# Kernel tuning notes

Measured on AMD Instinct MI355X. Metric: run time of the kernel, lower is better.

Reference implementation:

```python
import jax, jax.numpy as jnp
import numpy as np

B = 131072      # tokens routed (e.g., 16 seqs x 8192 tokens)
D_MODEL = 768
N_EXPERTS = 8
TOP_K = 2


def setup_inputs() -> dict:
    key = jax.random.key(0)
    k_h, k_w, k_b = jax.random.split(key, 3)
    h = jax.random.normal(k_h, (B, D_MODEL), dtype=jnp.float32)
    gate_w = jax.random.normal(k_w, (N_EXPERTS, D_MODEL), dtype=jnp.float32) * 0.02
    gate_b = jax.random.normal(k_b, (N_EXPERTS,), dtype=jnp.float32) * 0.02
    return {"h": h, "gate_w": gate_w, "gate_b": gate_b}


def reference(h, gate_w, gate_b):
    # gate projection: [B, d_model] @ [d_model, n_experts] + bias -> [B, n_experts]
    logits = jnp.einsum("bd,ed->be", h, gate_w) + gate_b
    # top-k selection (values, indices), then softmax over the top-k logits
    topk_vals, topk_idx = jax.lax.top_k(logits, TOP_K)   # [B, top_k] each
    weights = jax.nn.softmax(topk_vals, axis=-1)          # [B, top_k]
    return (topk_idx, weights)
```

## Files before the change

### kernel.cpp

```cpp
#include <hip/hip_runtime.h>


#define B_TOKENS 131072
#define DM 768
#define NE 8
#define TAU 1e-4f

__global__ __launch_bounds__(256) void router_main(
    const float* __restrict__ h,
    const float* __restrict__ gw,
    const float* __restrict__ gb,
    float* __restrict__ out,
    unsigned char* __restrict__ flags)
{
    const int lane = threadIdx.x & 63;
    const int wid = (blockIdx.x * blockDim.x + threadIdx.x) >> 6;
    const int n_waves = (gridDim.x * blockDim.x) >> 6;

    float wf[NE][3][4];
#pragma unroll
    for (int e = 0; e < NE; ++e)
#pragma unroll
        for (int g = 0; g < 3; ++g) {
            const float4 v = *reinterpret_cast<const float4*>(
                &gw[e * DM + g * 256 + lane * 4]);
            wf[e][g][0] = v.x; wf[e][g][1] = v.y;
            wf[e][g][2] = v.z; wf[e][g][3] = v.w;
        }

    float biasf[NE];
#pragma unroll
    for (int e = 0; e < NE; ++e) biasf[e] = gb[e];

    const bool hi32 = (lane & 32) != 0;
    const bool hi16 = (lane & 16) != 0;
    const bool hi8  = (lane & 8)  != 0;

    for (int t = wid; t < B_TOKENS; t += n_waves) {
        const float* hr = h + (size_t)t * DM;
        float4 buf[3];
#pragma unroll
        for (int g = 0; g < 3; ++g)
            buf[g] = *reinterpret_cast<const float4*>(&hr[g * 256 + lane * 4]);

        float accf[NE] = {0, 0, 0, 0, 0, 0, 0, 0};
#pragma unroll
        for (int g = 0; g < 3; ++g) {
            const float* bp = reinterpret_cast<const float*>(&buf[g]);
#pragma unroll
            for (int j = 0; j < 4; ++j) {
                const float hv = bp[j];
#pragma unroll
                for (int e = 0; e < NE; ++e)
                    accf[e] = fmaf(hv, wf[e][g][j], accf[e]);
            }
        }

        float r4[4];
#pragma unroll
        for (int j = 0; j < 4; ++j) {
            const float give = hi32 ? accf[j] : accf[4 + j];
            const float keep = hi32 ? accf[4 + j] : accf[j];
            r4[j] = keep + __shfl_xor(give, 32);
        }
        float r2[2];
#pragma unroll
        for (int j = 0; j < 2; ++j) {
            const float give = hi16 ? r4[j] : r4[2 + j];
            const float keep = hi16 ? r4[2 + j] : r4[j];
            r2[j] = keep + __shfl_xor(give, 16);
        }
        const float give = hi8 ? r2[0] : r2[1];
        const float keep = hi8 ? r2[1] : r2[0];
        float v = keep + __shfl_xor(give, 8);
        v += __shfl_xor(v, 4);
        v += __shfl_xor(v, 2);
        v += __shfl_xor(v, 1);

        float lg[NE];
#pragma unroll
        for (int e = 0; e < NE; ++e)
            lg[e] = __shfl(v, (e << 3) | (lane & 7)) + biasf[e];

        int i0 = 0; float v0 = lg[0];
#pragma unroll
        for (int e = 1; e < NE; ++e)
            if (lg[e] > v0) { v0 = lg[e]; i0 = e; }
        int i1 = -1; float v1 = -3.4e38f;
#pragma unroll
        for (int e = 0; e < NE; ++e)
            if (e != i0 && lg[e] > v1) { v1 = lg[e]; i1 = e; }
        float v2 = -3.4e38f;
#pragma unroll
        for (int e = 0; e < NE; ++e)
            if (e != i0 && e != i1 && lg[e] > v2) v2 = lg[e];

        const bool amb = (v0 - v1 < TAU) || (v1 - v2 < TAU);

        const float ex = expf(v1 - v0);
        const float w1 = ex / (1.0f + ex);
        const float w0 = 1.0f - w1;

        if (lane == 0) {
            *reinterpret_cast<float2*>(&out[2 * (size_t)t]) =
                make_float2((float)i0, (float)i1);
            *reinterpret_cast<float2*>(
                &out[2 * (size_t)B_TOKENS + 2 * (size_t)t]) =
                make_float2(w0, w1);
            flags[t] = amb ? 1 : 0;
        }
    }
}

__global__ __launch_bounds__(256) void router_repair(
    const float* __restrict__ h,
    const float* __restrict__ gw,
    const float* __restrict__ gb,
    float* __restrict__ out,
    const unsigned char* __restrict__ flags)
{
    const int lane = threadIdx.x & 63;
    const int w = (blockIdx.x * blockDim.x + threadIdx.x) >> 6;
    const int t0 = w * 64;
    if (t0 >= B_TOKENS) return;

    const unsigned char f = flags[t0 + lane];
    unsigned long long mask = __ballot(f != 0);
    if (mask == 0ull) return;

    float wf[NE][3][4];
#pragma unroll
    for (int e = 0; e < NE; ++e)
#pragma unroll
        for (int g = 0; g < 3; ++g) {
            const float4 vv = *reinterpret_cast<const float4*>(
                &gw[e * DM + g * 256 + lane * 4]);
            wf[e][g][0] = vv.x; wf[e][g][1] = vv.y;
            wf[e][g][2] = vv.z; wf[e][g][3] = vv.w;
        }
    double biasd[NE];
#pragma unroll
    for (int e = 0; e < NE; ++e) biasd[e] = (double)gb[e];

    const bool hi32 = (lane & 32) != 0;
    const bool hi16 = (lane & 16) != 0;
    const bool hi8  = (lane & 8)  != 0;

    while (mask) {
        const int p = __ffsll(mask) - 1;
        mask &= (mask - 1);
        const int t = t0 + p;

        const float* hr = h + (size_t)t * DM;
        float4 buf[3];
#pragma unroll
        for (int g = 0; g < 3; ++g)
            buf[g] = *reinterpret_cast<const float4*>(&hr[g * 256 + lane * 4]);

        double acc[NE] = {0, 0, 0, 0, 0, 0, 0, 0};
#pragma unroll
        for (int g = 0; g < 3; ++g) {
            const float* bp = reinterpret_cast<const float*>(&buf[g]);
#pragma unroll
            for (int j = 0; j < 4; ++j) {
                const double hd = (double)bp[j];
#pragma unroll
                for (int e = 0; e < NE; ++e)
                    acc[e] = fma(hd, (double)wf[e][g][j], acc[e]);
            }
        }
        double d4[4];
#pragma unroll
        for (int j = 0; j < 4; ++j) {
            const double give = hi32 ? acc[j] : acc[4 + j];
            const double keep = hi32 ? acc[4 + j] : acc[j];
            d4[j] = keep + __shfl_xor(give, 32);
        }
        double d2[2];
#pragma unroll
        for (int j = 0; j < 2; ++j) {
            const double give = hi16 ? d4[j] : d4[2 + j];
            const double keep = hi16 ? d4[2 + j] : d4[j];
            d2[j] = keep + __shfl_xor(give, 16);
        }
        const double give = hi8 ? d2[0] : d2[1];
        const double keep = hi8 ? d2[1] : d2[0];
        double dv = keep + __shfl_xor(give, 8);
        dv += __shfl_xor(dv, 4);
        dv += __shfl_xor(dv, 2);
        dv += __shfl_xor(dv, 1);

        double dlg[NE];
#pragma unroll
        for (int e = 0; e < NE; ++e)
            dlg[e] = __shfl(dv, (e << 3) | (lane & 7)) + biasd[e];

        int i0 = 0; double dv0 = dlg[0];
#pragma unroll
        for (int e = 1; e < NE; ++e)
            if (dlg[e] > dv0) { dv0 = dlg[e]; i0 = e; }
        int i1 = (i0 == 0) ? 1 : 0; double dv1 = dlg[i1];
#pragma unroll
        for (int e = 0; e < NE; ++e)
            if (e != i0 && dlg[e] > dv1) { dv1 = dlg[e]; i1 = e; }

        const float ex = expf((float)(dv1 - dv0));
        const float w1 = ex / (1.0f + ex);
        const float w0 = 1.0f - w1;

        if (lane == 0) {
            *reinterpret_cast<float2*>(&out[2 * (size_t)t]) =
                make_float2((float)i0, (float)i1);
            *reinterpret_cast<float2*>(
                &out[2 * (size_t)B_TOKENS + 2 * (size_t)t]) =
                make_float2(w0, w1);
        }
    }
}

extern "C" void kernel_launch(void* const* d_in, const int* in_sizes, int n_in,
                              void* d_out, int out_size, void* d_ws, size_t ws_size,
                              hipStream_t stream) {
    const float* h  = (const float*)d_in[0];
    const float* gw = (const float*)d_in[1];
    const float* gb = (const float*)d_in[2];
    float* out = (float*)d_out;
    unsigned char* flags = (unsigned char*)d_ws;

    router_main<<<dim3(2048), dim3(256), 0, stream>>>(h, gw, gb, out, flags);
    router_repair<<<dim3(512), dim3(256), 0, stream>>>(h, gw, gb, out, flags);
}
```

Baseline: 103.9 us.

## Restructure router to one token per thread with async LDS triple-buffered loads

The main kernel now assigns one token per thread instead of one token per wave. Each block streams its 256 token rows through a triple-buffered LDS ring using global_load_lds DMA, and gate weights are staged in LDS. Because each thread holds a token's full dot products, the cross-lane shuffle reductions are gone and every thread writes its own output. This adds a large LDS footprint (about 60KB), which limits occupancy, plus per-chunk barriers, and relies on hand-written vmcnt waits being correct.

```diff
diff --git a/kernel.cpp b/kernel.cpp
--- a/kernel.cpp
+++ b/kernel.cpp
@@ -5,6 +5,17 @@
 #define DM 768
 #define NE 8
 #define TAU 1e-4f
+#define TPB 256
+#define CH 12
+#define NCH 64
+#define HBUF 3072
+
+typedef const __attribute__((address_space(1))) void* gbl_vp;
+typedef __attribute__((address_space(3))) void* lds_vp;
+
+__device__ __forceinline__ void dma16(const float* g, float* l) {
+    __builtin_amdgcn_global_load_lds((gbl_vp)g, (lds_vp)l, 16, 0, 0);
+}
 
 __global__ __launch_bounds__(256) void router_main(
     const float* __restrict__ h,
@@ -13,103 +24,109 @@
     float* __restrict__ out,
     unsigned char* __restrict__ flags)
 {
-    const int lane = threadIdx.x & 63;
-    const int wid = (blockIdx.x * blockDim.x + threadIdx.x) >> 6;
-    const int n_waves = (gridDim.x * blockDim.x) >> 6;
-
-    float wf[NE][3][4];
+    __shared__ __align__(16) float w_lds[NE * DM];
+    __shared__ __align__(16) float h_lds[3 * HBUF];
+
+    const int tid  = threadIdx.x;
+    const int lane = tid & 63;
+    const int wv   = __builtin_amdgcn_readfirstlane(tid >> 6);
+    const int tb   = blockIdx.x * TPB;
+
+    const float* src[3];
+#pragma unroll
+    for (int i = 0; i < 3; ++i) {
+        const int sigma = wv * 192 + i * 64 + lane;
+        const int r = sigma / 3, g = sigma % 3;
+        src[i] = h + (size_t)(tb + r) * DM + g * 4;
+    }
+    const int dstoff0 = wv * 768;
+
+    dma16(src[0], &h_lds[0 * HBUF + dstoff0 + 0]);
+    dma16(src[1], &h_lds[0 * HBUF + dstoff0 + 256]);
+    dma16(src[2], &h_lds[0 * HBUF + dstoff0 + 512]);
+#pragma unroll
+    for (int i = 0; i < 3; ++i)
+        dma16(src[i] + CH, &h_lds[1 * HBUF + dstoff0 + i * 256]);
+#pragma unroll
+    for (int i = 0; i < 3; ++i) src[i] += 2 * CH;
+
+#pragma unroll
+    for (int s = 0; s < 6; ++s) {
+        const float4 v = *reinterpret_cast<const float4*>(&gw[(tid + s * TPB) * 4]);
+        *reinterpret_cast<float4*>(&w_lds[(tid + s * TPB) * 4]) = v;
+    }
+    float bias[NE];
+#pragma unroll
+    for (int e = 0; e < NE; ++e) bias[e] = gb[e];
+
+    __syncthreads();
+
+    float acc[NE] = {0, 0, 0, 0, 0, 0, 0, 0};
+
+    for (int k = 0; k < NCH; ++k) {
+        if (k == NCH - 1) {
+            asm volatile("s_waitcnt vmcnt(0)" ::: "memory");
+        } else {
+            asm volatile("s_waitcnt vmcnt(3)" ::: "memory");
+        }
+        __builtin_amdgcn_s_barrier();
+        __builtin_amdgcn_sched_barrier(0);
+
+        if (k + 2 < NCH) {
+            float* dst = &h_lds[((k + 2) % 3) * HBUF + dstoff0];
+            dma16(src[0], dst);
+            dma16(src[1], dst + 256);
+            dma16(src[2], dst + 512);
+#pragma unroll
+            for (int i = 0; i < 3; ++i) src[i] += CH;
+        }
+        __builtin_amdgcn_sched_barrier(0);
+
+        const float* row = &h_lds[(k % 3) * HBUF + tid * CH];
+        const int wbase = k * CH;
+#pragma unroll
+        for (int g2 = 0; g2 < 3; ++g2) {
+            const float4 hv = *reinterpret_cast<const float4*>(&row[g2 * 4]);
+#pragma unroll
+            for (int e = 0; e < NE; ++e) {
+                const float4 wv4 = *reinterpret_cast<const float4*>(
+                    &w_lds[e * DM + wbase + g2 * 4]);
+                acc[e] = fmaf(hv.x, wv4.x, acc[e]);
+                acc[e] = fmaf(hv.y, wv4.y, acc[e]);
+                acc[e] = fmaf(hv.z, wv4.z, acc[e]);
+                acc[e] = fmaf(hv.w, wv4.w, acc[e]);
+            }
+        }
+    }
+
+    float lg[NE];
+#pragma unroll
+    for (int e = 0; e < NE; ++e) lg[e] = acc[e] + bias[e];
+
+    int i0 = 0; float v0 = lg[0];
+#pragma unroll
+    for (int e = 1; e < NE; ++e)
+        if (lg[e] > v0) { v0 = lg[e]; i0 = e; }
+    int i1 = -1; float v1 = -3.4e38f;
 #pragma unroll
     for (int e = 0; e < NE; ++e)
-#pragma unroll
-        for (int g = 0; g < 3; ++g) {
-            const float4 v = *reinterpret_cast<const float4*>(
-                &gw[e * DM + g * 256 + lane * 4]);
-            wf[e][g][0] = v.x; wf[e][g][1] = v.y;
-            wf[e][g][2] = v.z; wf[e][g][3] = v.w;
-        }
-
-    float biasf[NE];
-#pragma unroll
-    for (int e = 0; e < NE; ++e) biasf[e] = gb[e];
-
-    const bool hi32 = (lane & 32) != 0;
-    const bool hi16 = (lane & 16) != 0;
-    const bool hi8  = (lane & 8)  != 0;
-
-    for (int t = wid; t < B_TOKENS; t += n_waves) {
-        const float* hr = h + (size_t)t * DM;
-        float4 buf[3];
-#pragma unroll
-        for (int g = 0; g < 3; ++g)
-            buf[g] = *reinterpret_cast<const float4*>(&hr[g * 256 + lane * 4]);
-
-        float accf[NE] = {0, 0, 0, 0, 0, 0, 0, 0};
-#pragma unroll
-        for (int g = 0; g < 3; ++g) {
-            const float* bp = reinterpret_cast<const float*>(&buf[g]);
-#pragma unroll
-            for (int j = 0; j < 4; ++j) {
-                const float hv = bp[j];
-#pragma unroll
-                for (int e = 0; e < NE; ++e)
-                    accf[e] = fmaf(hv, wf[e][g][j], accf[e]);
-            }
-        }
-
-        float r4[4];
-#pragma unroll
-        for (int j = 0; j < 4; ++j) {
-            const float give = hi32 ? accf[j] : accf[4 + j];
-            const float keep = hi32 ? accf[4 + j] : accf[j];
-            r4[j] = keep + __shfl_xor(give, 32);
-        }
-        float r2[2];
-#pragma unroll
-        for (int j = 0; j < 2; ++j) {
-            const float give = hi16 ? r4[j] : r4[2 + j];
-            const float keep = hi16 ? r4[2 + j] : r4[j];
-            r2[j] = keep + __shfl_xor(give, 16);
-        }
-        const float give = hi8 ? r2[0] : r2[1];
-        const float keep = hi8 ? r2[1] : r2[0];
-        float v = keep + __shfl_xor(give, 8);
-        v += __shfl_xor(v, 4);
-        v += __shfl_xor(v, 2);
-        v += __shfl_xor(v, 1);
-
-        float lg[NE];
-#pragma unroll
-        for (int e = 0; e < NE; ++e)
-            lg[e] = __shfl(v, (e << 3) | (lane & 7)) + biasf[e];
-
-        int i0 = 0; float v0 = lg[0];
-#pragma unroll
-        for (int e = 1; e < NE; ++e)
-            if (lg[e] > v0) { v0 = lg[e]; i0 = e; }
-        int i1 = -1; float v1 = -3.4e38f;
-#pragma unroll
-        for (int e = 0; e < NE; ++e)
-            if (e != i0 && lg[e] > v1) { v1 = lg[e]; i1 = e; }
-        float v2 = -3.4e38f;
-#pragma unroll
-        for (int e = 0; e < NE; ++e)
-            if (e != i0 && e != i1 && lg[e] > v2) v2 = lg[e];
-
-        const bool amb = (v0 - v1 < TAU) || (v1 - v2 < TAU);
-
-        const float ex = expf(v1 - v0);
-        const float w1 = ex / (1.0f + ex);
-        const float w0 = 1.0f - w1;
-
-        if (lane == 0) {
-            *reinterpret_cast<float2*>(&out[2 * (size_t)t]) =
-                make_float2((float)i0, (float)i1);
-            *reinterpret_cast<float2*>(
-                &out[2 * (size_t)B_TOKENS + 2 * (size_t)t]) =
-                make_float2(w0, w1);
-            flags[t] = amb ? 1 : 0;
-        }
-    }
+        if (e != i0 && lg[e] > v1) { v1 = lg[e]; i1 = e; }
+    float v2 = -3.4e38f;
+#pragma unroll
+    for (int e = 0; e < NE; ++e)
+        if (e != i0 && e != i1 && lg[e] > v2) v2 = lg[e];
+
+    const bool amb = (v0 - v1 < TAU) || (v1 - v2 < TAU);
+
+    const float ex = expf(v1 - v0);
+    const float w1 = ex / (1.0f + ex);
+    const float w0 = 1.0f - w1;
+
+    const size_t t = (size_t)(tb + tid);
+    *reinterpret_cast<float2*>(&out[2 * t]) = make_float2((float)i0, (float)i1);
+    *reinterpret_cast<float2*>(&out[2 * (size_t)B_TOKENS + 2 * t]) =
+        make_float2(w0, w1);
+    flags[t] = amb ? 1 : 0;
 }
 
 __global__ __launch_bounds__(256) void router_repair(
@@ -227,6 +244,6 @@
     float* out = (float*)d_out;
     unsigned char* flags = (unsigned char*)d_ws;
 
-    router_main<<<dim3(2048), dim3(256), 0, stream>>>(h, gw, gb, out, flags);
+    router_main<<<dim3(B_TOKENS / TPB), dim3(TPB), 0, stream>>>(h, gw, gb, out, flags);
     router_repair<<<dim3(512), dim3(256), 0, stream>>>(h, gw, gb, out, flags);
 }
```

Result: slower. 136.2 us (+31.0%).

## Prefetch token rows into LDS with async global_load_lds triple buffering

Applied to the files above, without the earlier changes.

The main router kernel now streams each wave's token rows into a three-slot LDS ring using global_load_lds DMA. Loads run three tokens ahead and are gated by explicit vmcnt waits, so memory latency overlaps the FMA and reduction work. The grid is halved to 1024 blocks and each wave handles exactly 32 tokens at a fixed stride. The hand-written waitcnt and sched_barrier sequencing is fragile, adds 36KB of LDS per block, and the fixed token mapping hardcodes the grid size.

```diff
diff --git a/kernel.cpp b/kernel.cpp
--- a/kernel.cpp
+++ b/kernel.cpp
@@ -5,6 +5,15 @@
 #define DM 768
 #define NE 8
 #define TAU 1e-4f
+#define NWAVES 4096
+#define NT 32
+
+typedef const __attribute__((address_space(1))) void* gbl_vp;
+typedef __attribute__((address_space(3))) void* lds_vp;
+
+__device__ __forceinline__ void dma16(const float* g, float* l) {
+    __builtin_amdgcn_global_load_lds((gbl_vp)g, (lds_vp)l, 16, 0, 0);
+}
 
 __global__ __launch_bounds__(256) void router_main(
     const float* __restrict__ h,
@@ -13,47 +22,76 @@
     float* __restrict__ out,
     unsigned char* __restrict__ flags)
 {
-    const int lane = threadIdx.x & 63;
-    const int wid = (blockIdx.x * blockDim.x + threadIdx.x) >> 6;
-    const int n_waves = (gridDim.x * blockDim.x) >> 6;
-
-    float wf[NE][3][4];
+    __shared__ __align__(16) float hslots[4][3][DM];
+
+    const int tid  = threadIdx.x;
+    const int lane = tid & 63;
+    const int wv   = __builtin_amdgcn_readfirstlane(tid >> 6);
+    const int wid  = blockIdx.x * 4 + (tid >> 6);
+
+    float4 wf[NE][3];
 #pragma unroll
     for (int e = 0; e < NE; ++e)
 #pragma unroll
-        for (int g = 0; g < 3; ++g) {
-            const float4 v = *reinterpret_cast<const float4*>(
+        for (int g = 0; g < 3; ++g)
+            wf[e][g] = *reinterpret_cast<const float4*>(
                 &gw[e * DM + g * 256 + lane * 4]);
-            wf[e][g][0] = v.x; wf[e][g][1] = v.y;
-            wf[e][g][2] = v.z; wf[e][g][3] = v.w;
-        }
 
     float biasf[NE];
 #pragma unroll
     for (int e = 0; e < NE; ++e) biasf[e] = gb[e];
+
+#pragma unroll
+    for (int kk = 0; kk < 3; ++kk) {
+        const float* row = h + (size_t)(wid + kk * NWAVES) * DM;
+#pragma unroll
+        for (int i = 0; i < 3; ++i)
+            dma16(row + i * 256 + lane * 4, &hslots[wv][kk][i * 256]);
+    }
 
     const bool hi32 = (lane & 32) != 0;
     const bool hi16 = (lane & 16) != 0;
     const bool hi8  = (lane & 8)  != 0;
 
-    for (int t = wid; t < B_TOKENS; t += n_waves) {
-        const float* hr = h + (size_t)t * DM;
-        float4 buf[3];
-#pragma unroll
-        for (int g = 0; g < 3; ++g)
-            buf[g] = *reinterpret_cast<const float4*>(&hr[g * 256 + lane * 4]);
+    for (int k = 0; k < NT; ++k) {
+        const int t = wid + k * NWAVES;
+
+        if (k <= NT - 3)      asm volatile("s_waitcnt vmcnt(6)" ::: "memory");
+        else if (k == NT - 2) asm volatile("s_waitcnt vmcnt(3)" ::: "memory");
+        else                  asm volatile("s_waitcnt vmcnt(0)" ::: "memory");
+
+        const float* slot = &hslots[wv][k % 3][0];
+        const float4 h0 = *reinterpret_cast<const float4*>(&slot[0 + lane * 4]);
+        const float4 h1 = *reinterpret_cast<const float4*>(&slot[256 + lane * 4]);
+        const float4 h2 = *reinterpret_cast<const float4*>(&slot[512 + lane * 4]);
+
+        asm volatile("s_waitcnt lgkmcnt(0)" ::: "memory");
+        __builtin_amdgcn_sched_barrier(0);
+
+        if (k + 3 < NT) {
+            const float* row = h + (size_t)(t + 3 * NWAVES) * DM;
+            float* dst = &hslots[wv][k % 3][0];
+#pragma unroll
+            for (int i = 0; i < 3; ++i)
+                dma16(row + i * 256 + lane * 4, dst + i * 256);
+        }
+        __builtin_amdgcn_sched_barrier(0);
 
         float accf[NE] = {0, 0, 0, 0, 0, 0, 0, 0};
 #pragma unroll
-        for (int g = 0; g < 3; ++g) {
-            const float* bp = reinterpret_cast<const float*>(&buf[g]);
-#pragma unroll
-            for (int j = 0; j < 4; ++j) {
-                const float hv = bp[j];
-#pragma unroll
-                for (int e = 0; e < NE; ++e)
-                    accf[e] = fmaf(hv, wf[e][g][j], accf[e]);
-            }
+        for (int e = 0; e < NE; ++e) {
+            accf[e] = fmaf(h0.x, wf[e][0].x, accf[e]);
+            accf[e] = fmaf(h0.y, wf[e][0].y, accf[e]);
+            accf[e] = fmaf(h0.z, wf[e][0].z, accf[e]);
+            accf[e] = fmaf(h0.w, wf[e][0].w, accf[e]);
+            accf[e] = fmaf(h1.x, wf[e][1].x, accf[e]);
+            accf[e] = fmaf(h1.y, wf[e][1].y, accf[e]);
+            accf[e] = fmaf(h1.z, wf[e][1].z, accf[e]);
+            accf[e] = fmaf(h1.w, wf[e][1].w, accf[e]);
+            accf[e] = fmaf(h2.x, wf[e][2].x, accf[e]);
+            accf[e] = fmaf(h2.y, wf[e][2].y, accf[e]);
+            accf[e] = fmaf(h2.z, wf[e][2].z, accf[e]);
+            accf[e] = fmaf(h2.w, wf[e][2].w, accf[e]);
         }
 
         float r4[4];
@@ -227,6 +265,6 @@
     float* out = (float*)d_out;
     unsigned char* flags = (unsigned char*)d_ws;
 
-    router_main<<<dim3(2048), dim3(256), 0, stream>>>(h, gw, gb, out, flags);
+    router_main<<<dim3(1024), dim3(256), 0, stream>>>(h, gw, gb, out, flags);
     router_repair<<<dim3(512), dim3(256), 0, stream>>>(h, gw, gb, out, flags);
 }
```

Result: slower. 118.3 us (+13.8%).

## Compute gate logits with split-bf16 MFMA and shuffle-based top-k

Applied to the files above, without the earlier changes.

Replaces the per-wave-per-token FMA dot product with tiles of 16 tokens per wave computed by MFMA 16x16x32 bf16 instructions. To keep near-fp32 accuracy, both activations and weights are split into hi/lo bf16 parts and three MFMAs are issued per k-step. Gate weights are pre-split into LDS. Top-2 and the third value are found with butterfly shuffles and ballots, and the ambiguity threshold is widened so the fp64 repair kernel handles more borderline tokens. This trades vector FMA work and per-token reductions for matrix-core throughput, at the cost of extra conversion ALU work, reduced precision, and a larger repair workload.

```diff
diff --git a/kernel.cpp b/kernel.cpp
--- a/kernel.cpp
+++ b/kernel.cpp
@@ -1,10 +1,23 @@
 #include <hip/hip_runtime.h>
+#include <hip/hip_bf16.h>
 
 
 #define B_TOKENS 131072
 #define DM 768
 #define NE 8
-#define TAU 1e-4f
+#define TAU 2.5e-4f
+#define NEG_BIG -3.0e38f
+
+typedef __attribute__((ext_vector_type(8))) short bf16x8;
+typedef __attribute__((ext_vector_type(4))) float f32x4;
+
+__device__ __forceinline__ unsigned short f32_to_bf16(float f) {
+    __hip_bfloat16 b = __float2bfloat16(f);
+    return *reinterpret_cast<unsigned short*>(&b);
+}
+__device__ __forceinline__ float bf16_to_f32(unsigned short u) {
+    return __uint_as_float((unsigned)u << 16);
+}
 
 __global__ __launch_bounds__(256) void router_main(
     const float* __restrict__ h,
@@ -13,99 +26,96 @@
     float* __restrict__ out,
     unsigned char* __restrict__ flags)
 {
-    const int lane = threadIdx.x & 63;
-    const int wid = (blockIdx.x * blockDim.x + threadIdx.x) >> 6;
-    const int n_waves = (gridDim.x * blockDim.x) >> 6;
-
-    float wf[NE][3][4];
-#pragma unroll
-    for (int e = 0; e < NE; ++e)
-#pragma unroll
-        for (int g = 0; g < 3; ++g) {
-            const float4 v = *reinterpret_cast<const float4*>(
-                &gw[e * DM + g * 256 + lane * 4]);
-            wf[e][g][0] = v.x; wf[e][g][1] = v.y;
-            wf[e][g][2] = v.z; wf[e][g][3] = v.w;
-        }
-
-    float biasf[NE];
-#pragma unroll
-    for (int e = 0; e < NE; ++e) biasf[e] = gb[e];
-
-    const bool hi32 = (lane & 32) != 0;
-    const bool hi16 = (lane & 16) != 0;
-    const bool hi8  = (lane & 8)  != 0;
-
-    for (int t = wid; t < B_TOKENS; t += n_waves) {
-        const float* hr = h + (size_t)t * DM;
-        float4 buf[3];
-#pragma unroll
-        for (int g = 0; g < 3; ++g)
-            buf[g] = *reinterpret_cast<const float4*>(&hr[g * 256 + lane * 4]);
-
-        float accf[NE] = {0, 0, 0, 0, 0, 0, 0, 0};
-#pragma unroll
-        for (int g = 0; g < 3; ++g) {
-            const float* bp = reinterpret_cast<const float*>(&buf[g]);
-#pragma unroll
-            for (int j = 0; j < 4; ++j) {
-                const float hv = bp[j];
-#pragma unroll
-                for (int e = 0; e < NE; ++e)
-                    accf[e] = fmaf(hv, wf[e][g][j], accf[e]);
+    __shared__ __align__(16) unsigned short w_lds[24 * 576 + 8];
+
+    const int tid  = threadIdx.x;
+    const int lane = tid & 63;
+    const int wv   = tid >> 6;
+    const int col  = lane & 15;
+    const int kg   = lane >> 4;
+
+    for (int idx = tid; idx < NE * DM; idx += 256) {
+        const int e = idx / DM, k = idx - e * DM;
+        const float w = gw[idx];
+        const unsigned short hb = f32_to_bf16(w);
+        const unsigned short lb = f32_to_bf16(w - bf16_to_f32(hb));
+        const int ks = k >> 5, kk = k & 31;
+        w_lds[ks * 576 + e * 72 + kk]      = hb;
+        w_lds[ks * 576 + e * 72 + 32 + kk] = lb;
+    }
+    if (tid < 8) w_lds[24 * 576 + tid] = 0;
+
+    const float bias_lane = (col < 8) ? gb[col] : NEG_BIG;
+    __syncthreads();
+
+    const int tile = blockIdx.x * 4 + wv;
+    const float* arow = h + (size_t)(tile * 16 + col) * DM + kg * 8;
+
+    const unsigned short* bptr =
+        (col < 8) ? &w_lds[col * 72 + kg * 8] : &w_lds[24 * 576];
+    const int bstep = (col < 8) ? 576 : 0;
+    const int bloff = (col < 8) ? 32 : 0;
+
+    f32x4 acc = {0.f, 0.f, 0.f, 0.f};
+#pragma unroll 4
+    for (int ks = 0; ks < 24; ++ks) {
+        const float4 p = *reinterpret_cast<const float4*>(arow + ks * 32);
+        const float4 q = *reinterpret_cast<const float4*>(arow + ks * 32 + 4);
+        bf16x8 ahi, alo;
+        {
+            const float fv[8] = {p.x, p.y, p.z, p.w, q.x, q.y, q.z, q.w};
+#pragma unroll
+            for (int j = 0; j < 8; ++j) {
+                const unsigned short hb = f32_to_bf16(fv[j]);
+                const unsigned short lb = f32_to_bf16(fv[j] - bf16_to_f32(hb));
+                ahi[j] = (short)hb;
+                alo[j] = (short)lb;
             }
         }
-
-        float r4[4];
-#pragma unroll
-        for (int j = 0; j < 4; ++j) {
-            const float give = hi32 ? accf[j] : accf[4 + j];
-            const float keep = hi32 ? accf[4 + j] : accf[j];
-            r4[j] = keep + __shfl_xor(give, 32);
-        }
-        float r2[2];
-#pragma unroll
-        for (int j = 0; j < 2; ++j) {
-            const float give = hi16 ? r4[j] : r4[2 + j];
-            const float keep = hi16 ? r4[2 + j] : r4[j];
-            r2[j] = keep + __shfl_xor(give, 16);
-        }
-        const float give = hi8 ? r2[0] : r2[1];
-        const float keep = hi8 ? r2[1] : r2[0];
-        float v = keep + __shfl_xor(give, 8);
-        v += __shfl_xor(v, 4);
-        v += __shfl_xor(v, 2);
-        v += __shfl_xor(v, 1);
-
-        float lg[NE];
-#pragma unroll
-        for (int e = 0; e < NE; ++e)
-            lg[e] = __shfl(v, (e << 3) | (lane & 7)) + biasf[e];
-
-        int i0 = 0; float v0 = lg[0];
-#pragma unroll
-        for (int e = 1; e < NE; ++e)
-            if (lg[e] > v0) { v0 = lg[e]; i0 = e; }
-        int i1 = -1; float v1 = -3.4e38f;
-#pragma unroll
-        for (int e = 0; e < NE; ++e)
-            if (e != i0 && lg[e] > v1) { v1 = lg[e]; i1 = e; }
-        float v2 = -3.4e38f;
-#pragma unroll
-        for (int e = 0; e < NE; ++e)
-            if (e != i0 && e != i1 && lg[e] > v2) v2 = lg[e];
-
-        const bool amb = (v0 - v1 < TAU) || (v1 - v2 < TAU);
-
-        const float ex = expf(v1 - v0);
-        const float w1 = ex / (1.0f + ex);
-        const float w0 = 1.0f - w1;
-
-        if (lane == 0) {
-            *reinterpret_cast<float2*>(&out[2 * (size_t)t]) =
+        const bf16x8 bhi = *reinterpret_cast<const bf16x8*>(bptr + ks * bstep);
+        const bf16x8 blo = *reinterpret_cast<const bf16x8*>(bptr + ks * bstep + bloff);
+        acc = __builtin_amdgcn_mfma_f32_16x16x32_bf16(ahi, bhi, acc, 0, 0, 0);
+        acc = __builtin_amdgcn_mfma_f32_16x16x32_bf16(ahi, blo, acc, 0, 0, 0);
+        acc = __builtin_amdgcn_mfma_f32_16x16x32_bf16(alo, bhi, acc, 0, 0, 0);
+    }
+
+    const unsigned gsh = (unsigned)(lane & 48);
+#pragma unroll
+    for (int i = 0; i < 4; ++i) {
+        const float lg = acc[i] + bias_lane;
+        float a0 = lg, a1 = NEG_BIG, a2 = NEG_BIG;
+#pragma unroll
+        for (int m = 1; m <= 4; m <<= 1) {
+            const float b0 = __shfl_xor(a0, m);
+            const float b1 = __shfl_xor(a1, m);
+            const float b2 = __shfl_xor(a2, m);
+            const float x  = fminf(a0, b0);
+            const float c0 = fmaxf(a0, b0);
+            const float y  = fmaxf(a1, b1);
+            const float z  = fminf(a1, b1);
+            const float c1 = fmaxf(x, y);
+            const float c2 = fmaxf(fminf(x, y), fmaxf(z, fmaxf(a2, b2)));
+            a0 = c0; a1 = c1; a2 = c2;
+        }
+        const unsigned long long m0 = __ballot(lg == a0);
+        const unsigned long long m1 = __ballot(lg == a1);
+        const unsigned mk0 = (unsigned)(m0 >> gsh) & 0xFFu;
+        const unsigned mk1 = (unsigned)(m1 >> gsh) & 0xFFu;
+        const int i0 = __builtin_ctz(mk0);
+        const unsigned rest = mk0 & (mk0 - 1);
+        const int i1 = (a1 == a0) ? __builtin_ctz(rest | 0x100u)
+                                  : __builtin_ctz(mk1 | 0x100u);
+
+        const bool amb = (a0 - a1 < TAU) || (a1 - a2 < TAU);
+        const float ex = expf(a1 - a0);
+        const float w1 = ex / (1.f + ex);
+        const float w0 = 1.f - w1;
+
+        if (col == 0) {
+            const size_t t = (size_t)(tile * 16 + (lane >> 4) * 4 + i);
+            *reinterpret_cast<float2*>(&out[2 * t]) =
                 make_float2((float)i0, (float)i1);
-            *reinterpret_cast<float2*>(
-                &out[2 * (size_t)B_TOKENS + 2 * (size_t)t]) =
+            *reinterpret_cast<float2*>(&out[2 * (size_t)B_TOKENS + 2 * t]) =
                 make_float2(w0, w1);
             flags[t] = amb ? 1 : 0;
         }
@@ -147,7 +157,7 @@
     const bool hi8  = (lane & 8)  != 0;
 
     while (mask) {
-        const int p = __ffsll(mask) - 1;
+        const int p = __ffsll((unsigned long long)mask) - 1;
         mask &= (mask - 1);
         const int t = t0 + p;
 
```

After: 88.89 us. 14.5% less time.
